# Kernel tuning notes

Hardware: AMD Instinct MI355X
Metric: run time of the kernel (lower is better)

Reference implementation:

```python
import jax, jax.numpy as jnp
import numpy as np

N = 16384  # number of internal DAG nodes
L = 16384  # number of leaves


def setup_inputs() -> dict:
    key = jax.random.key(0)
    ks = jax.random.split(key, 12)
    idx = jnp.arange(N)
    # internal-child offsets and leaf ids
    off_l = jax.random.randint(ks[0], (N,), 1, N)
    off_r = jax.random.randint(ks[1], (N,), 1, N)
    leaf_l = jax.random.randint(ks[2], (N,), 0, L)
    leaf_r = jax.random.randint(ks[3], (N,), 0, L)
    is_int_l = (jax.random.uniform(ks[4], (N,)) < 0.5) & (idx < N - 1)
    is_int_r = (jax.random.uniform(ks[5], (N,)) < 0.5) & (idx < N - 1)
    # forward-pointing DAG: internal child index strictly greater than parent
    left = jnp.where(is_int_l, jnp.clip(idx + off_l, 0, N - 1), -(leaf_l + 1)).astype(jnp.int32)
    right = jnp.where(is_int_r, jnp.clip(idx + off_r, 0, N - 1), -(leaf_r + 1)).astype(jnp.int32)
    return {
        "thresholds": jax.random.normal(ks[6], (N,), dtype=jnp.float32),
        "rules": jax.random.randint(ks[7], (N,), 0, 16).astype(jnp.int32),
        "binary_ops": jax.random.randint(ks[8], (N,), 0, 8).astype(jnp.int32),
        "left": left,
        "right": right,
        "leaf_is_reroll": jax.random.uniform(ks[9], (L,)) < 0.5,
        "leaf_mask_left": jax.random.randint(ks[10], (L,), 0, 64).astype(jnp.int32),
        "leaf_mask_right": jax.random.randint(ks[11], (L,), 0, 64).astype(jnp.int32),
        "leaf_mask_op": jax.random.randint(jax.random.fold_in(key, 100), (L,), 0, 4).astype(jnp.int32),
        "leaf_score_cat": jax.random.randint(jax.random.fold_in(key, 101), (L,), 0, 16).astype(jnp.int32),
    }


def _active_mask(left, right, n_nodes):
    def step(reachable, _):
        active_left = jnp.where(reachable & (left >= 0), left, n_nodes)
        active_right = jnp.where(reachable & (right >= 0), right, n_nodes)
        new_reachable = jnp.zeros(n_nodes + 1, dtype=jnp.bool_)
        new_reachable = new_reachable.at[active_left].set(True)
        new_reachable = new_reachable.at[active_right].set(True)
        new_reachable = new_reachable.at[0].set(True)
        return new_reachable[:n_nodes] | reachable, None

    init = jnp.zeros(n_nodes, dtype=jnp.bool_).at[0].set(True)
    mask, _ = jax.lax.scan(step, init, None, length=n_nodes)
    return mask


def _subtree_leaf_flags(left, right, leaf_is_reroll, n):
    def is_leaf_score(child):
        leaf_id = -child - 1
        return (child < 0) & (~leaf_is_reroll[leaf_id])

    def is_leaf_reroll(child):
        leaf_id = -child - 1
        return (child < 0) & leaf_is_reroll[leaf_id]

    def step(carry, i):
        has_score, has_reroll = carry
        node = n - 1 - i  # postorder: children have larger indices
        l, r = left[node], right[node]

        def child_has_score(child):
            return is_leaf_score(child) | jnp.where(child >= 0, has_score[child], False)

        def child_has_reroll(child):
            return is_leaf_reroll(child) | jnp.where(child >= 0, has_reroll[child], False)

        has_score = has_score.at[node].set(child_has_score(l) | child_has_score(r))
        has_reroll = has_reroll.at[node].set(child_has_reroll(l) | child_has_reroll(r))
        return (has_score, has_reroll), None

    init = (jnp.zeros(n, dtype=jnp.bool_), jnp.zeros(n, dtype=jnp.bool_))
    (has_score, has_reroll), _ = jax.lax.scan(step, init, jnp.arange(n))
    return has_score, has_reroll


def reference(thresholds, rules, binary_ops, left, right, leaf_is_reroll,
              leaf_mask_left, leaf_mask_right, leaf_mask_op, leaf_score_cat):
    n = rules.shape[0]
    active_mask = _active_mask(left, right, n)
    has_score, has_reroll = _subtree_leaf_flags(left, right, leaf_is_reroll, n)
    active_node_count = jnp.sum(active_mask)
    return active_mask, has_score, has_reroll, active_node_count
```

## Files before the change

### kernel.cpp

```cpp
#include <hip/hip_runtime.h>

#define NN 16384
#define NT 1024
#define PER 16

__global__ __launch_bounds__(NT) void dag_eval_kernel(
    const int* __restrict__ left,
    const int* __restrict__ right,
    const unsigned char* __restrict__ reroll_raw,
    int* __restrict__ out)
{
    __shared__ unsigned char reach[NN];
    __shared__ unsigned char state[NN + 16];
    __shared__ int flags[2];
    __shared__ int nzmask;
    __shared__ int cnt;

    const int tid = threadIdx.x;
    const int b0  = tid * PER;

    if (tid == 0) { nzmask = 0; cnt = 0; flags[0] = 0; flags[1] = 0; }
    if (tid < 16) state[NN + tid] = 0;

    int lch[PER], rch[PER];
    {
        const int4* l4 = (const int4*)left;
        const int4* r4 = (const int4*)right;
        #pragma unroll
        for (int j = 0; j < PER / 4; ++j) {
            int4 a = l4[(b0 >> 2) + j];
            int4 b = r4[(b0 >> 2) + j];
            lch[4*j+0] = a.x; lch[4*j+1] = a.y; lch[4*j+2] = a.z; lch[4*j+3] = a.w;
            rch[4*j+0] = b.x; rch[4*j+1] = b.y; rch[4*j+2] = b.z; rch[4*j+3] = b.w;
        }
    }

    {
        uint4 v = ((const uint4*)reroll_raw)[tid];
        unsigned int t = v.x | v.y | v.z | v.w;
        unsigned int m = 0;
        if (t & 0x000000FFu) m |= 1u;
        if (t & 0x0000FF00u) m |= 2u;
        if (t & 0x00FF0000u) m |= 4u;
        if (t & 0xFF000000u) m |= 8u;
        if (m) atomicOr(&nzmask, (int)m);
    }

    *(uint4*)&reach[b0] = make_uint4(0u, 0u, 0u, 0u);
    __syncthreads();

    const int mask   = nzmask;
    const int layout = ((mask & ~1) == 0) ? 0 : (((mask & 3) == 0) ? 1 : 2);
    const int*   ri = (const int*)reroll_raw;
    const float* rf = (const float*)reroll_raw;

    int sreg[PER];
    #pragma unroll
    for (int k = 0; k < PER; ++k) {
        int s = 0;
        int c = lch[k];
        if (c < 0) {
            int id = -c - 1;
            bool rr = (layout == 2) ? (reroll_raw[id] != 0)
                     : (layout == 1) ? (rf[id] != 0.0f)
                                     : (ri[id] != 0);
            s |= rr ? 2 : 1;
        }
        c = rch[k];
        if (c < 0) {
            int id = -c - 1;
            bool rr = (layout == 2) ? (reroll_raw[id] != 0)
                     : (layout == 1) ? (rf[id] != 0.0f)
                                     : (ri[id] != 0);
            s |= rr ? 2 : 1;
        }
        sreg[k] = s;
        state[b0 + k] = (unsigned char)s;
    }
    if (tid == 0) reach[0] = 1;
    __syncthreads();

    unsigned int pushed = 0, mm = 0;
    for (int s = 0; ; ++s) {
        uint4 rv = *(const uint4*)&reach[b0];
        mm  =  ((rv.x * 0x01020408u) >> 24) & 0xFu;
        mm |= (((rv.y * 0x01020408u) >> 24) & 0xFu) << 4;
        mm |= (((rv.z * 0x01020408u) >> 24) & 0xFu) << 8;
        mm |= (((rv.w * 0x01020408u) >> 24) & 0xFu) << 12;
        unsigned int newp = mm & ~pushed;
        pushed |= newp;
        const bool ch = (newp != 0u);
        while (newp) {
            int k = __builtin_ctz(newp);
            newp &= newp - 1u;
            int c = lch[k]; if (c >= 0) reach[c] = (unsigned char)1;
            c = rch[k];     if (c >= 0) reach[c] = (unsigned char)1;
        }
        int p = s & 1;
        if (ch) flags[p] = 1;
        __syncthreads();
        int f = flags[p];
        if (tid == 0) flags[p ^ 1] = 0;
        __syncthreads();
        if (!f) break;
    }

    unsigned int unres = 0;
    #pragma unroll
    for (int k = 0; k < PER; ++k) if (sreg[k] != 3) unres |= 1u << k;

    for (int s = 0; ; ++s) {
        bool ch = false;
        if (unres) {
            int tl[PER], tr[PER];
            #pragma unroll
            for (int k = 0; k < PER; ++k) {
                bool act = (unres >> k) & 1u;
                int la = (act && lch[k] >= 0) ? lch[k] : NN;
                int ra = (act && rch[k] >= 0) ? rch[k] : NN;
                tl[k] = state[la];
                tr[k] = state[ra];
            }
            #pragma unroll
            for (int k = 0; k < PER; ++k) {
                int ns = sreg[k] | tl[k] | tr[k];
                if (ns != sreg[k]) {
                    sreg[k] = ns;
                    state[b0 + k] = (unsigned char)ns;
                    ch = true;
                    if (ns == 3) unres &= ~(1u << k);
                }
            }
        }
        int p = s & 1;
        if (ch) flags[p] = 1;
        __syncthreads();
        int f = flags[p];
        if (tid == 0) flags[p ^ 1] = 0;
        __syncthreads();
        if (!f) break;
    }

    int cc = __popc(mm);
    #pragma unroll
    for (int off = 32; off; off >>= 1) cc += __shfl_down(cc, off);
    if ((tid & 63) == 0) atomicAdd(&cnt, cc);

    int4* out4 = (int4*)out;
    #pragma unroll
    for (int j = 0; j < PER / 4; ++j) {
        int4 a, h, r;
        a.x = (mm >> (4*j+0)) & 1; a.y = (mm >> (4*j+1)) & 1;
        a.z = (mm >> (4*j+2)) & 1; a.w = (mm >> (4*j+3)) & 1;
        h.x =  sreg[4*j+0] & 1;       h.y =  sreg[4*j+1] & 1;
        h.z =  sreg[4*j+2] & 1;       h.w =  sreg[4*j+3] & 1;
        r.x = (sreg[4*j+0] >> 1) & 1; r.y = (sreg[4*j+1] >> 1) & 1;
        r.z = (sreg[4*j+2] >> 1) & 1; r.w = (sreg[4*j+3] >> 1) & 1;
        out4[(b0 >> 2) + j]              = a;
        out4[((NN + b0) >> 2) + j]       = h;
        out4[((2 * NN + b0) >> 2) + j]   = r;
    }
    __syncthreads();
    if (tid == 0) out[3 * NN] = cnt;
}

extern "C" void kernel_launch(void* const* d_in, const int* in_sizes, int n_in,
                              void* d_out, int out_size, void* d_ws, size_t ws_size,
                              hipStream_t stream)
{
    const int* left  = (const int*)d_in[3];
    const int* right = (const int*)d_in[4];
    const unsigned char* reroll = (const unsigned char*)d_in[5];
    int* out = (int*)d_out;
    dag_eval_kernel<<<1, NT, 0, stream>>>(left, right, reroll, out);
}
```

Measured before the change: 32.30 us.

## Fuse reachability and leaf-flag propagation with windowed local iterations and finalized bits

Measured after the change: 39.28 us. 21.6% more time.

```diff
diff --git a/kernel.cpp b/kernel.cpp
--- a/kernel.cpp
+++ b/kernel.cpp
@@ -3,6 +3,7 @@
 #define NN 16384
 #define NT 1024
 #define PER 16
+#define KWIN 4
 
 __global__ __launch_bounds__(NT) void dag_eval_kernel(
     const int* __restrict__ left,
@@ -20,7 +21,7 @@
     const int b0  = tid * PER;
 
     if (tid == 0) { nzmask = 0; cnt = 0; flags[0] = 0; flags[1] = 0; }
-    if (tid < 16) state[NN + tid] = 0;
+    if (tid < 16) state[NN + tid] = 4;
 
     int lch[PER], rch[PER];
     {
@@ -55,25 +56,27 @@
     const float* rf = (const float*)reroll_raw;
 
     int sreg[PER];
+    unsigned int todo = 0;
     #pragma unroll
     for (int k = 0; k < PER; ++k) {
         int s = 0;
-        int c = lch[k];
-        if (c < 0) {
-            int id = -c - 1;
+        int l = lch[k], r = rch[k];
+        if (l < 0) {
+            int id = -l - 1;
             bool rr = (layout == 2) ? (reroll_raw[id] != 0)
                      : (layout == 1) ? (rf[id] != 0.0f)
                                      : (ri[id] != 0);
             s |= rr ? 2 : 1;
         }
-        c = rch[k];
-        if (c < 0) {
-            int id = -c - 1;
+        if (r < 0) {
+            int id = -r - 1;
             bool rr = (layout == 2) ? (reroll_raw[id] != 0)
                      : (layout == 1) ? (rf[id] != 0.0f)
                                      : (ri[id] != 0);
             s |= rr ? 2 : 1;
         }
+        if ((l < 0 && r < 0) || s == 3) s |= 4;
+        else todo |= 1u << k;
         sreg[k] = s;
         state[b0 + k] = (unsigned char)s;
     }
@@ -81,58 +84,57 @@
     __syncthreads();
 
     unsigned int pushed = 0, mm = 0;
-    for (int s = 0; ; ++s) {
-        uint4 rv = *(const uint4*)&reach[b0];
-        mm  =  ((rv.x * 0x01020408u) >> 24) & 0xFu;
-        mm |= (((rv.y * 0x01020408u) >> 24) & 0xFu) << 4;
-        mm |= (((rv.z * 0x01020408u) >> 24) & 0xFu) << 8;
-        mm |= (((rv.w * 0x01020408u) >> 24) & 0xFu) << 12;
-        unsigned int newp = mm & ~pushed;
-        pushed |= newp;
-        const bool ch = (newp != 0u);
-        while (newp) {
-            int k = __builtin_ctz(newp);
-            newp &= newp - 1u;
-            int c = lch[k]; if (c >= 0) reach[c] = (unsigned char)1;
-            c = rch[k];     if (c >= 0) reach[c] = (unsigned char)1;
-        }
-        int p = s & 1;
-        if (ch) flags[p] = 1;
-        __syncthreads();
-        int f = flags[p];
-        if (tid == 0) flags[p ^ 1] = 0;
-        __syncthreads();
-        if (!f) break;
-    }
-
-    unsigned int unres = 0;
-    #pragma unroll
-    for (int k = 0; k < PER; ++k) if (sreg[k] != 3) unres |= 1u << k;
-
-    for (int s = 0; ; ++s) {
+    for (int w = 0; ; ++w) {
         bool ch = false;
-        if (unres) {
-            int tl[PER], tr[PER];
-            #pragma unroll
-            for (int k = 0; k < PER; ++k) {
-                bool act = (unres >> k) & 1u;
-                int la = (act && lch[k] >= 0) ? lch[k] : NN;
-                int ra = (act && rch[k] >= 0) ? rch[k] : NN;
-                tl[k] = state[la];
-                tr[k] = state[ra];
+        for (int it = 0; it < KWIN; ++it) {
+            bool c2 = false;
+            uint4 rv = *(const uint4*)&reach[b0];
+            mm  =  ((rv.x * 0x01020408u) >> 24) & 0xFu;
+            mm |= (((rv.y * 0x01020408u) >> 24) & 0xFu) << 4;
+            mm |= (((rv.z * 0x01020408u) >> 24) & 0xFu) << 8;
+            mm |= (((rv.w * 0x01020408u) >> 24) & 0xFu) << 12;
+            unsigned int newp = mm & ~pushed;
+            pushed |= newp;
+            if (newp) c2 = true;
+            while (newp) {
+                int k = __builtin_ctz(newp);
+                newp &= newp - 1u;
+                int c = lch[k]; if (c >= 0) reach[c] = (unsigned char)1;
+                c = rch[k];     if (c >= 0) reach[c] = (unsigned char)1;
             }
-            #pragma unroll
-            for (int k = 0; k < PER; ++k) {
-                int ns = sreg[k] | tl[k] | tr[k];
-                if (ns != sreg[k]) {
-                    sreg[k] = ns;
-                    state[b0 + k] = (unsigned char)ns;
-                    ch = true;
-                    if (ns == 3) unres &= ~(1u << k);
+            if (todo) {
+                int tl[PER], tr[PER];
+                #pragma unroll
+                for (int k = 0; k < PER; ++k) {
+                    bool act = (todo >> k) & 1u;
+                    int la = (act && lch[k] >= 0) ? lch[k] : NN;
+                    int ra = (act && rch[k] >= 0) ? rch[k] : NN;
+                    tl[k] = state[la];
+                    tr[k] = state[ra];
+                }
+                #pragma unroll
+                for (int k = 0; k < PER; ++k) {
+                    if ((todo >> k) & 1u) {
+                        int sl = tl[k], sr = tr[k];
+                        int ns = sreg[k] | (sl & 3) | (sr & 3);
+                        if (((sl & sr) & 4) || (ns & 3) == 3) {
+                            ns |= 4;
+                            todo &= ~(1u << k);
+                            sreg[k] = ns;
+                            state[b0 + k] = (unsigned char)ns;
+                            c2 = true;
+                        } else if (ns != sreg[k]) {
+                            sreg[k] = ns;
+                            state[b0 + k] = (unsigned char)ns;
+                            c2 = true;
+                        }
+                    }
                 }
             }
+            ch |= c2;
+            if (!c2) break;
         }
-        int p = s & 1;
+        int p = w & 1;
         if (ch) flags[p] = 1;
         __syncthreads();
         int f = flags[p];
```

## Replace barrier-driven fixpoints with single-wave BFS and wave-chained subtree propagation

Applied to the files above, without the earlier changes.

After: 67.03 us. 2.08x slower.

```diff
diff --git a/kernel.cpp b/kernel.cpp
--- a/kernel.cpp
+++ b/kernel.cpp
@@ -3,6 +3,7 @@
 #define NN 16384
 #define NT 1024
 #define PER 16
+#define QCAP 2048
 
 __global__ __launch_bounds__(NT) void dag_eval_kernel(
     const int* __restrict__ left,
@@ -10,28 +11,52 @@
     const unsigned char* __restrict__ reroll_raw,
     int* __restrict__ out)
 {
-    __shared__ unsigned char reach[NN];
-    __shared__ unsigned char state[NN + 16];
-    __shared__ int flags[2];
+    __shared__ __align__(16) unsigned int  pairs[NN];
+    __shared__ __align__(16) unsigned char state[NN + 16];
+    __shared__ __align__(16) unsigned char reach[NN];
+    __shared__ __align__(16) unsigned char rbits[NN / 8];
+    __shared__ unsigned short q[2][QCAP];
+    __shared__ int readyB[16];
     __shared__ int nzmask;
     __shared__ int cnt;
 
-    const int tid = threadIdx.x;
-    const int b0  = tid * PER;
-
-    if (tid == 0) { nzmask = 0; cnt = 0; flags[0] = 0; flags[1] = 0; }
-    if (tid < 16) state[NN + tid] = 0;
-
-    int lch[PER], rch[PER];
+    const int tid  = threadIdx.x;
+    const int w    = tid >> 6;
+    const int lane = tid & 63;
+
+    if (tid < 16) { readyB[tid] = 0; state[NN + tid] = 4; }
+    if (tid == 0) { nzmask = 0; cnt = 0; }
+
     {
         const int4* l4 = (const int4*)left;
         const int4* r4 = (const int4*)right;
+        const int base = tid * PER;
         #pragma unroll
         for (int j = 0; j < PER / 4; ++j) {
-            int4 a = l4[(b0 >> 2) + j];
-            int4 b = r4[(b0 >> 2) + j];
-            lch[4*j+0] = a.x; lch[4*j+1] = a.y; lch[4*j+2] = a.z; lch[4*j+3] = a.w;
-            rch[4*j+0] = b.x; rch[4*j+1] = b.y; rch[4*j+2] = b.z; rch[4*j+3] = b.w;
+            int4 a = l4[(base >> 2) + j];
+            int4 b = r4[(base >> 2) + j];
+            uint4 pk;
+            pk.x = (a.x & 0xFFFF) | ((unsigned)b.x << 16);
+            pk.y = (a.y & 0xFFFF) | ((unsigned)b.y << 16);
+            pk.z = (a.z & 0xFFFF) | ((unsigned)b.z << 16);
+            pk.w = (a.w & 0xFFFF) | ((unsigned)b.w << 16);
+            *(uint4*)&pairs[base + 4 * j] = pk;
+        }
+    }
+
+    const int own_base = (15 - w) * 1024 + lane * PER;
+    unsigned int cpair[PER];
+    {
+        const int4* l4 = (const int4*)left;
+        const int4* r4 = (const int4*)right;
+        #pragma unroll
+        for (int j = 0; j < PER / 4; ++j) {
+            int4 a = l4[(own_base >> 2) + j];
+            int4 b = r4[(own_base >> 2) + j];
+            cpair[4*j+0] = (a.x & 0xFFFF) | ((unsigned)b.x << 16);
+            cpair[4*j+1] = (a.y & 0xFFFF) | ((unsigned)b.y << 16);
+            cpair[4*j+2] = (a.z & 0xFFFF) | ((unsigned)b.z << 16);
+            cpair[4*j+3] = (a.w & 0xFFFF) | ((unsigned)b.w << 16);
         }
     }
 
@@ -45,120 +70,148 @@
         if (t & 0xFF000000u) m |= 8u;
         if (m) atomicOr(&nzmask, (int)m);
     }
-
-    *(uint4*)&reach[b0] = make_uint4(0u, 0u, 0u, 0u);
-    __syncthreads();
-
-    const int mask   = nzmask;
-    const int layout = ((mask & ~1) == 0) ? 0 : (((mask & 3) == 0) ? 1 : 2);
-    const int*   ri = (const int*)reroll_raw;
-    const float* rf = (const float*)reroll_raw;
+    *(uint4*)&reach[tid * PER] = make_uint4(0u, 0u, 0u, 0u);
+    __syncthreads();
+
+    {
+        const bool bytelay = (nzmask == 0xF) || (nzmask == 0);
+        unsigned int m16 = 0;
+        if (bytelay) {
+            uint4 v = ((const uint4*)reroll_raw)[tid];
+            unsigned int wd[4] = {v.x, v.y, v.z, v.w};
+            #pragma unroll
+            for (int j = 0; j < 4; ++j)
+                #pragma unroll
+                for (int b = 0; b < 4; ++b)
+                    if ((wd[j] >> (8 * b)) & 0xFFu) m16 |= 1u << (4 * j + b);
+        } else {
+            const uint4* p = (const uint4*)reroll_raw;
+            #pragma unroll
+            for (int j = 0; j < 4; ++j) {
+                uint4 v = p[tid * 4 + j];
+                if (v.x) m16 |= 1u << (4 * j + 0);
+                if (v.y) m16 |= 1u << (4 * j + 1);
+                if (v.z) m16 |= 1u << (4 * j + 2);
+                if (v.w) m16 |= 1u << (4 * j + 3);
+            }
+        }
+        ((unsigned short*)rbits)[tid] = (unsigned short)m16;
+    }
+    if (tid == 0) { reach[0] = 1; q[0][0] = 0; }
+    __syncthreads();
 
     int sreg[PER];
-    #pragma unroll
-    for (int k = 0; k < PER; ++k) {
-        int s = 0;
-        int c = lch[k];
-        if (c < 0) {
-            int id = -c - 1;
-            bool rr = (layout == 2) ? (reroll_raw[id] != 0)
-                     : (layout == 1) ? (rf[id] != 0.0f)
-                                     : (ri[id] != 0);
-            s |= rr ? 2 : 1;
-        }
-        c = rch[k];
-        if (c < 0) {
-            int id = -c - 1;
-            bool rr = (layout == 2) ? (reroll_raw[id] != 0)
-                     : (layout == 1) ? (rf[id] != 0.0f)
-                                     : (ri[id] != 0);
-            s |= rr ? 2 : 1;
-        }
-        sreg[k] = s;
-        state[b0 + k] = (unsigned char)s;
-    }
-    if (tid == 0) reach[0] = 1;
-    __syncthreads();
-
-    unsigned int pushed = 0, mm = 0;
-    for (int s = 0; ; ++s) {
-        uint4 rv = *(const uint4*)&reach[b0];
-        mm  =  ((rv.x * 0x01020408u) >> 24) & 0xFu;
-        mm |= (((rv.y * 0x01020408u) >> 24) & 0xFu) << 4;
-        mm |= (((rv.z * 0x01020408u) >> 24) & 0xFu) << 8;
-        mm |= (((rv.w * 0x01020408u) >> 24) & 0xFu) << 12;
-        unsigned int newp = mm & ~pushed;
-        pushed |= newp;
-        const bool ch = (newp != 0u);
-        while (newp) {
-            int k = __builtin_ctz(newp);
-            newp &= newp - 1u;
-            int c = lch[k]; if (c >= 0) reach[c] = (unsigned char)1;
-            c = rch[k];     if (c >= 0) reach[c] = (unsigned char)1;
-        }
-        int p = s & 1;
-        if (ch) flags[p] = 1;
-        __syncthreads();
-        int f = flags[p];
-        if (tid == 0) flags[p ^ 1] = 0;
-        __syncthreads();
-        if (!f) break;
-    }
-
     unsigned int unres = 0;
-    #pragma unroll
-    for (int k = 0; k < PER; ++k) if (sreg[k] != 3) unres |= 1u << k;
-
-    for (int s = 0; ; ++s) {
-        bool ch = false;
-        if (unres) {
-            int tl[PER], tr[PER];
-            #pragma unroll
-            for (int k = 0; k < PER; ++k) {
-                bool act = (unres >> k) & 1u;
-                int la = (act && lch[k] >= 0) ? lch[k] : NN;
-                int ra = (act && rch[k] >= 0) ? rch[k] : NN;
-                tl[k] = state[la];
-                tr[k] = state[ra];
+    {
+        unsigned int sw[4] = {0, 0, 0, 0};
+        #pragma unroll
+        for (int k = 0; k < PER; ++k) {
+            int c0 = (int)(short)(cpair[k] & 0xFFFF);
+            int c1 = (int)(short)(cpair[k] >> 16);
+            int s = 0;
+            if (c0 < 0) { int id = -c0 - 1; s |= ((rbits[id >> 3] >> (id & 7)) & 1) ? 2 : 1; }
+            if (c1 < 0) { int id = -c1 - 1; s |= ((rbits[id >> 3] >> (id & 7)) & 1) ? 2 : 1; }
+            if ((c0 < 0 && c1 < 0) || s == 3) s |= 4;
+            else unres |= 1u << k;
+            sreg[k] = s;
+            sw[k >> 2] |= (unsigned)s << (8 * (k & 3));
+        }
+        *(uint4*)&state[own_base] = make_uint4(sw[0], sw[1], sw[2], sw[3]);
+    }
+    __syncthreads();
+
+    volatile int* rB = readyB;
+
+    if (w == 15) {
+        int cur = 0, cn = 1;
+        int safety = 600;
+        while (cn > 0 && --safety) {
+            int nn2 = 0;
+            for (int base = 0; base < cn; base += 64) {
+                int idx = base + lane;
+                bool act = idx < cn;
+                int node = act ? (int)q[cur][idx] : 0;
+                unsigned int pr = pairs[node];
+                int c0 = (int)(short)(pr & 0xFFFF);
+                int c1 = (int)(short)(pr >> 16);
+                bool p0 = act && c0 > 0 && reach[c0] == 0;
+                bool p1 = act && c1 > 0 && reach[c1] == 0;
+                if (p0) reach[c0] = (unsigned char)1;
+                if (p1) reach[c1] = (unsigned char)1;
+                unsigned long long lt = (1ULL << lane) - 1ULL;
+                unsigned long long m0 = __ballot(p0);
+                if (p0) q[cur ^ 1][nn2 + __popcll(m0 & lt)] = (unsigned short)c0;
+                nn2 += __popcll(m0);
+                unsigned long long m1 = __ballot(p1);
+                if (p1) q[cur ^ 1][nn2 + __popcll(m1 & lt)] = (unsigned short)c1;
+                nn2 += __popcll(m1);
+                if (nn2 > QCAP - 64) nn2 = QCAP - 64;
+                asm volatile("" ::: "memory");
             }
-            #pragma unroll
-            for (int k = 0; k < PER; ++k) {
-                int ns = sreg[k] | tl[k] | tr[k];
-                if (ns != sreg[k]) {
-                    sreg[k] = ns;
-                    state[b0 + k] = (unsigned char)ns;
-                    ch = true;
-                    if (ns == 3) unres &= ~(1u << k);
-                }
+            cur ^= 1; cn = nn2;
+        }
+    }
+
+    if (w > 0) {
+        int spins = 0;
+        while (rB[w - 1] == 0 && spins < (1 << 17)) { ++spins; __builtin_amdgcn_s_sleep(1); }
+    }
+    asm volatile("" ::: "memory");
+    while (__any(unres != 0)) {
+        #pragma unroll
+        for (int k = 0; k < PER; ++k) {
+            if ((unres >> k) & 1u) {
+                int c0 = (int)(short)(cpair[k] & 0xFFFF);
+                int c1 = (int)(short)(cpair[k] >> 16);
+                int la = (c0 > 0) ? c0 : NN;
+                int ra = (c1 > 0) ? c1 : NN;
+                int sl = state[la];
+                int sr = state[ra];
+                int ns = sreg[k] | (sl & 3) | (sr & 3);
+                bool fin = ((sl & sr & 4) != 0) || ((ns & 3) == 3);
+                if (fin) { ns |= 4; unres &= ~(1u << k); }
+                if (ns != sreg[k]) { sreg[k] = ns; state[own_base + k] = (unsigned char)ns; }
             }
         }
-        int p = s & 1;
-        if (ch) flags[p] = 1;
-        __syncthreads();
-        int f = flags[p];
-        if (tid == 0) flags[p ^ 1] = 0;
-        __syncthreads();
-        if (!f) break;
-    }
-
-    int cc = __popc(mm);
-    #pragma unroll
-    for (int off = 32; off; off >>= 1) cc += __shfl_down(cc, off);
-    if ((tid & 63) == 0) atomicAdd(&cnt, cc);
+        asm volatile("" ::: "memory");
+    }
+    __threadfence_block();
+    if (lane == 0) rB[w] = 1;
+
+    __syncthreads();
+
+    {
+        uint4 v = *(const uint4*)&reach[tid * PER];
+        unsigned int t = v.x + v.y + v.z + v.w;
+        int cc = (t & 0xFF) + ((t >> 8) & 0xFF) + ((t >> 16) & 0xFF) + (t >> 24);
+        #pragma unroll
+        for (int off = 32; off; off >>= 1) cc += __shfl_down(cc, off);
+        if (lane == 0) atomicAdd(&cnt, cc);
+    }
 
     int4* out4 = (int4*)out;
+    {
+        uint4 v = *(const uint4*)&reach[tid * PER];
+        unsigned int wd[4] = {v.x, v.y, v.z, v.w};
+        #pragma unroll
+        for (int j = 0; j < 4; ++j) {
+            int4 a;
+            a.x = (wd[j] >> 0)  & 1;
+            a.y = (wd[j] >> 8)  & 1;
+            a.z = (wd[j] >> 16) & 1;
+            a.w = (wd[j] >> 24) & 1;
+            out4[(tid * PER >> 2) + j] = a;
+        }
+    }
     #pragma unroll
     for (int j = 0; j < PER / 4; ++j) {
-        int4 a, h, r;
-        a.x = (mm >> (4*j+0)) & 1; a.y = (mm >> (4*j+1)) & 1;
-        a.z = (mm >> (4*j+2)) & 1; a.w = (mm >> (4*j+3)) & 1;
+        int4 h, r;
         h.x =  sreg[4*j+0] & 1;       h.y =  sreg[4*j+1] & 1;
         h.z =  sreg[4*j+2] & 1;       h.w =  sreg[4*j+3] & 1;
         r.x = (sreg[4*j+0] >> 1) & 1; r.y = (sreg[4*j+1] >> 1) & 1;
         r.z = (sreg[4*j+2] >> 1) & 1; r.w = (sreg[4*j+3] >> 1) & 1;
-        out4[(b0 >> 2) + j]              = a;
-        out4[((NN + b0) >> 2) + j]       = h;
-        out4[((2 * NN + b0) >> 2) + j]   = r;
+        out4[((NN + own_base) >> 2) + j]     = h;
+        out4[((2 * NN + own_base) >> 2) + j] = r;
     }
     __syncthreads();
     if (tid == 0) out[3 * NN] = cnt;
```
